# Optimization experiments

Measured on AMD Instinct MI355X. Metric: run time of the kernel, lower is better.

## Reference

```python
import jax, jax.numpy as jnp
import numpy as np

NCLS = 6
K = 2
ATOMS = 5          # ('vm','im','cm','sc','cc')
IN_DIM = 768
HID = 3072
NUM_PATCH = 576
B = 64
# Task t gates over 6 experts: [dense expert 0] + 5 atom-pair experts (a_in=t%5, a_out=0..4)
TASK_ATOM = [t % ATOMS for t in range(NCLS)]


def setup_inputs() -> dict:
    key = jax.random.key(0)
    ks = jax.random.split(key, 12)
    s = 0.02
    return {
        "x": jax.random.normal(ks[0], (B, NCLS + NUM_PATCH, IN_DIM), jnp.float32),
        "W1": jax.random.normal(ks[1], (IN_DIM, HID), jnp.float32) * s,
        "b1": jnp.zeros((HID,), jnp.float32),
        "W2": jax.random.normal(ks[2], (HID, IN_DIM), jnp.float32) * s,
        "b2": jnp.zeros((IN_DIM,), jnp.float32),
        "W_in": jax.random.normal(ks[3], (ATOMS, IN_DIM, HID), jnp.float32) * s,
        "b_in": jnp.zeros((ATOMS, HID), jnp.float32),
        "W_out": jax.random.normal(ks[4], (ATOMS, HID, IN_DIM), jnp.float32) * s,
        "b_out": jnp.zeros((ATOMS, IN_DIM), jnp.float32),
        "Wg": jax.random.normal(ks[5], (NCLS, IN_DIM, 6), jnp.float32) * s,
    }


def _gelu(x):
    return jax.nn.gelu(x, approximate=False)  # torch nn.GELU default (erf)


def reference(x, W1, b1, W2, b2, W_in, b_in, W_out, b_out, Wg):
    cls = x[:, :NCLS]                      # [B, ncls, d]
    patch = x[:, NCLS:]                    # [B, P, d]
    # dense FFN on patch tokens
    patch = _gelu(jnp.einsum('bpd,dh->bph', patch, W1) + b1)
    patch = jnp.einsum('bph,hd->bpd', patch, W2) + b2

    flat = cls.reshape(-1, cls.shape[-1])  # [N=B*ncls, d]
    # expert 0: the same dense FFN
    e0 = (_gelu(flat @ W1 + b1) @ W2 + b2).reshape(B, NCLS, IN_DIM)
    # atom-pair experts: shared hidden per atom_in, then each atom_out head
    hid = _gelu(jnp.einsum('nd,adh->anh', flat, W_in) + b_in[:, None, :])       # [5, N, H]
    allo = jnp.einsum('anh,ohd->aond', hid, W_out) + b_out[None, :, None, :]    # [5, 5, N, d]
    allo = allo.reshape(ATOMS, ATOMS, B, NCLS, IN_DIM)

    rows = jnp.arange(B)[:, None]
    mixed = []
    for t in range(NCLS):
        a = TASK_ATOM[t]
        g = jax.nn.softmax(cls[:, t] @ Wg[t], axis=-1)            # [B, 6]
        vals, idx = jax.lax.top_k(g, K)
        sparse = jnp.zeros_like(g).at[rows, idx].set(vals)
        g = sparse / jnp.maximum(sparse.sum(-1, keepdims=True), 1e-6)
        # selected experts in index order: [0, (a,0)..(a,4)]
        sel = jnp.concatenate(
            [e0[:, t][:, None, :], jnp.swapaxes(allo[a, :, :, t, :], 0, 1)], axis=1
        )                                                          # [B, 6, d]
        mixed.append(jnp.sum(sel * g[:, :, None], axis=1, keepdims=True))
    cls_out = jnp.concatenate(mixed, axis=1)                       # [B, ncls, d]
    return jnp.concatenate([cls_out, patch], axis=1)  # dropout is identity in eval
```

## Files before the change

### kernel.cpp

```cpp
#include <hip/hip_runtime.h>
#include <math.h>


typedef unsigned short bfu;
typedef __attribute__((ext_vector_type(8))) short bf16x8;
typedef __attribute__((ext_vector_type(4))) float f32x4;

#define GLD_LDS16(g, l)                                                        \
  __builtin_amdgcn_global_load_lds(                                            \
      (const __attribute__((address_space(1))) void*)(g),                      \
      (__attribute__((address_space(3))) void*)(l), 16, 0, 0)

__device__ __forceinline__ bfu f2bf(float f) {
  unsigned int u = __float_as_uint(f);
  u += 0x7FFFu + ((u >> 16) & 1u);
  return (bfu)(u >> 16);
}
__device__ __forceinline__ float gelu_exact(float v) {
  return 0.5f * v * (1.0f + erff(v * 0.70710678118654752440f));
}

template <int BM, int WC, int MF, int NF, bool GELU, bool OUTBF>
__device__ __forceinline__ void gemm_tile(
    bfu* As, bfu* Bs,
    const bfu* __restrict__ A,
    const bfu* __restrict__ Bt,
    const float* __restrict__ bias,
    void* __restrict__ out,
    int K, int ldo) {
  const int tid  = threadIdx.x;
  const int lane = tid & 63;
  const int wv   = tid >> 6;
  const int wm   = (wv / WC) * (MF * 16);
  const int wn   = (wv % WC) * (NF * 16);

  const f32x4 fzero = {0.f, 0.f, 0.f, 0.f};
  f32x4 acc[MF][NF];
#pragma unroll
  for (int m = 0; m < MF; ++m)
#pragma unroll
    for (int n = 0; n < NF; ++n) acc[m][n] = fzero;

  const int srow  = tid >> 3;
  const int gslot = (tid & 7) ^ (srow & 7);
  const bfu* ga = A  + (size_t)srow * K + gslot * 8;
  const bfu* gb = Bt + (size_t)srow * K + gslot * 8;

  const int lrow = lane & 15;
  const int lks  = lane >> 4;

  for (int kt = 0; kt < K; kt += 64) {
#pragma unroll
    for (int i = 0; i < BM / 32; ++i)
      GLD_LDS16(ga + kt + (size_t)i * 32 * K, As + i * 2048 + wv * 512);
#pragma unroll
    for (int i = 0; i < 4; ++i)
      GLD_LDS16(gb + kt + (size_t)i * 32 * K, Bs + i * 2048 + wv * 512);
    __syncthreads();

#pragma unroll
    for (int kk = 0; kk < 2; ++kk) {
      bf16x8 af[MF], bfr[NF];
#pragma unroll
      for (int m = 0; m < MF; ++m) {
        int row  = wm + m * 16 + lrow;
        int slot = (kk * 4 + lks) ^ (row & 7);
        af[m] = *(const bf16x8*)(As + row * 64 + slot * 8);
      }
#pragma unroll
      for (int n = 0; n < NF; ++n) {
        int row  = wn + n * 16 + lrow;
        int slot = (kk * 4 + lks) ^ (row & 7);
        bfr[n] = *(const bf16x8*)(Bs + row * 64 + slot * 8);
      }
#pragma unroll
      for (int m = 0; m < MF; ++m)
#pragma unroll
        for (int n = 0; n < NF; ++n)
          acc[m][n] = __builtin_amdgcn_mfma_f32_16x16x32_bf16(af[m], bfr[n],
                                                              acc[m][n], 0, 0, 0);
    }
    __syncthreads();
  }

  const int rbase = (lane >> 4) * 4;
#pragma unroll
  for (int n = 0; n < NF; ++n) {
    int col = wn + n * 16 + lrow;
    float bv = bias[col];
#pragma unroll
    for (int m = 0; m < MF; ++m) {
#pragma unroll
      for (int r = 0; r < 4; ++r) {
        int row = wm + m * 16 + rbase + r;
        float v = acc[m][n][r] + bv;
        if (GELU) v = gelu_exact(v);
        if (OUTBF)
          ((bfu*)out)[(size_t)row * ldo + col] = f2bf(v);
        else
          ((float*)out)[(size_t)row * ldo + col] = v;
      }
    }
  }
}

template <bool GELU, bool OUTBF>
__global__ __launch_bounds__(256) void gemm128_kernel(
    const bfu* __restrict__ A, const bfu* __restrict__ Bt,
    const float* __restrict__ bias, void* __restrict__ out, int K, int ldo) {
  __shared__ bfu As[128 * 64];
  __shared__ bfu Bs[128 * 64];
  size_t m0 = (size_t)blockIdx.x * 128, n0 = (size_t)blockIdx.y * 128;
  gemm_tile<128, 2, 4, 4, GELU, OUTBF>(
      As, Bs, A + m0 * K, Bt + n0 * K, bias + n0,
      (void*)((char*)out + ((size_t)m0 * ldo + n0) * (OUTBF ? 2 : 4)), K, ldo);
}

__global__ __launch_bounds__(256) void hidc_kernel(
    const bfu* __restrict__ clsb, const bfu* __restrict__ WinT,
    const float* __restrict__ b_in, bfu* __restrict__ hidc) {
  __shared__ bfu As[64 * 64];
  __shared__ bfu Bs[128 * 64];
  int t = blockIdx.y, a = t % 5, nt = blockIdx.x;
  gemm_tile<64, 4, 4, 2, true, true>(
      As, Bs, clsb + (size_t)t * 64 * 768,
      WinT + (size_t)a * 3072 * 768 + (size_t)nt * 128 * 768,
      b_in + a * 3072 + nt * 128,
      (void*)(hidc + (size_t)t * 64 * 3072 + nt * 128), 768, 3072);
}

__global__ __launch_bounds__(256) void allo_kernel(
    const bfu* __restrict__ hidc, const bfu* __restrict__ WoutT,
    const float* __restrict__ b_out, float* __restrict__ allo) {
  __shared__ bfu As[64 * 64];
  __shared__ bfu Bs[128 * 64];
  int t = blockIdx.y, nt = blockIdx.x;
  gemm_tile<64, 4, 4, 2, false, false>(
      As, Bs, hidc + (size_t)t * 64 * 3072,
      WoutT + (size_t)nt * 128 * 3072, b_out + nt * 128,
      (void*)(allo + (size_t)t * 64 * 3840 + nt * 128), 3072, 3840);
}

__global__ __launch_bounds__(256) void cvt_f32_bf16_kernel(
    const float* __restrict__ in, bfu* __restrict__ out, int n4) {
  int stride = gridDim.x * blockDim.x;
  for (int i = blockIdx.x * blockDim.x + threadIdx.x; i < n4; i += stride) {
    float4 v = ((const float4*)in)[i];
    ushort4 o;
    o.x = f2bf(v.x); o.y = f2bf(v.y); o.z = f2bf(v.z); o.w = f2bf(v.w);
    ((ushort4*)out)[i] = o;
  }
}

__global__ __launch_bounds__(256) void transpose_kernel(
    const float* __restrict__ in, bfu* __restrict__ out, int R, int C) {
  __shared__ float tile[32][33];
  int z = blockIdx.z;
  const float* src = in + (size_t)z * R * C;
  bfu* dst = out + (size_t)z * R * C;
  int c0 = blockIdx.x * 32, r0 = blockIdx.y * 32;
  int tx = threadIdx.x, ty = threadIdx.y;
#pragma unroll
  for (int j = 0; j < 32; j += 8)
    tile[ty + j][tx] = src[(size_t)(r0 + ty + j) * C + c0 + tx];
  __syncthreads();
#pragma unroll
  for (int j = 0; j < 32; j += 8)
    dst[(size_t)(c0 + ty + j) * R + r0 + tx] = f2bf(tile[tx][ty + j]);
}

__global__ __launch_bounds__(256) void build_clsb_kernel(
    const float* __restrict__ x, bfu* __restrict__ clsb) {
  int i = blockIdx.x * 256 + threadIdx.x;
  int d = i % 768, bt = i / 768;
  int b = bt % 64, t = bt / 64;
  clsb[i] = f2bf(x[((size_t)b * 582 + t) * 768 + d]);
}

__global__ __launch_bounds__(64) void gate_kernel(
    const float* __restrict__ x, const float* __restrict__ Wg,
    float* __restrict__ gw) {
  int bt = blockIdx.x;
  int b = bt / 6, t = bt % 6;
  const float* xr = x + ((size_t)b * 582 + t) * 768;
  const float* wg = Wg + (size_t)t * 768 * 6;
  int lane = threadIdx.x;
  float z[6] = {0.f, 0.f, 0.f, 0.f, 0.f, 0.f};
  for (int d = lane; d < 768; d += 64) {
    float xv = xr[d];
#pragma unroll
    for (int o = 0; o < 6; ++o) z[o] += xv * wg[d * 6 + o];
  }
#pragma unroll
  for (int o = 0; o < 6; ++o)
#pragma unroll
    for (int s = 32; s > 0; s >>= 1) z[o] += __shfl_down(z[o], s);
  if (lane == 0) {
    int i1 = 0;
#pragma unroll
    for (int o = 1; o < 6; ++o) if (z[o] > z[i1]) i1 = o;
    int i2 = -1;
#pragma unroll
    for (int o = 0; o < 6; ++o) {
      if (o == i1) continue;
      if (i2 < 0 || z[o] > z[i2]) i2 = o;
    }
    float w1 = 1.f / (1.f + expf(z[i2] - z[i1]));
    float o6[6] = {0.f, 0.f, 0.f, 0.f, 0.f, 0.f};
    o6[i1] = w1; o6[i2] = 1.f - w1;
#pragma unroll
    for (int o = 0; o < 6; ++o) gw[bt * 6 + o] = o6[o];
  }
}

__global__ __launch_bounds__(256) void mix_kernel(
    float* __restrict__ out, const float* __restrict__ allo,
    const float* __restrict__ gw) {
  int bt = blockIdx.x;
  int b = bt / 6, t = bt % 6;
  float g[6];
#pragma unroll
  for (int o = 0; o < 6; ++o) g[o] = gw[bt * 6 + o];
  float* orow = out + ((size_t)b * 582 + t) * 768;
  const float* arow = allo + ((size_t)t * 64 + b) * 3840;
  for (int d = threadIdx.x; d < 768; d += 256) {
    float v = g[0] * orow[d];
#pragma unroll
    for (int o = 0; o < 5; ++o) v += g[o + 1] * arow[o * 768 + d];
    orow[d] = v;
  }
}

extern "C" void kernel_launch(void* const* d_in, const int* in_sizes, int n_in,
                              void* d_out, int out_size, void* d_ws,
                              size_t ws_size, hipStream_t stream) {
  const float* x     = (const float*)d_in[0];
  const float* W1    = (const float*)d_in[1];
  const float* b1    = (const float*)d_in[2];
  const float* W2    = (const float*)d_in[3];
  const float* b2    = (const float*)d_in[4];
  const float* W_in  = (const float*)d_in[5];
  const float* b_in  = (const float*)d_in[6];
  const float* W_out = (const float*)d_in[7];
  const float* b_out = (const float*)d_in[8];
  const float* Wg    = (const float*)d_in[9];
  float* out = (float*)d_out;

  constexpr int M = 37248;
  constexpr int CHUNK_TILES = 97;
  constexpr int CHUNK_ROWS  = CHUNK_TILES * 128;
  constexpr size_t SZ_XB    = (size_t)M * 768 * 2;
  constexpr size_t SZ_W1T   = (size_t)3072 * 768 * 2;
  constexpr size_t SZ_W2T   = (size_t)768 * 3072 * 2;
  constexpr size_t SZ_WINT  = (size_t)5 * 3072 * 768 * 2;
  constexpr size_t SZ_WOUTT = (size_t)5 * 768 * 3072 * 2;
  constexpr size_t SZ_HID   = (size_t)CHUNK_ROWS * 3072 * 2;
  constexpr size_t SZ_CLSB  = (size_t)6 * 64 * 768 * 2;
  constexpr size_t SZ_HIDC  = (size_t)6 * 64 * 3072 * 2;
  constexpr size_t SZ_ALLO  = (size_t)6 * 64 * 3840 * 4;
  constexpr size_t SZ_GW    = (size_t)384 * 6 * 4;

  char* ws = (char*)d_ws;
  size_t off = 0;
  auto take = [&](size_t bytes) {
    char* p = ws + off;
    off += (bytes + 255) & ~(size_t)255;
    return p;
  };
  bfu*   xb    = (bfu*)take(SZ_XB);
  bfu*   W1t   = (bfu*)take(SZ_W1T);
  bfu*   W2t   = (bfu*)take(SZ_W2T);
  bfu*   WinT  = (bfu*)take(SZ_WINT);
  bfu*   WoutT = (bfu*)take(SZ_WOUTT);
  bfu*   hid   = (bfu*)take(SZ_HID);
  bfu*   clsb  = (bfu*)take(SZ_CLSB);
  bfu*   hidc  = (bfu*)take(SZ_HIDC);
  float* allo  = (float*)take(SZ_ALLO);
  float* gw    = (float*)take(SZ_GW);
  if (ws_size < off) return;

  cvt_f32_bf16_kernel<<<2048, 256, 0, stream>>>(x, xb, M * 768 / 4);
  transpose_kernel<<<dim3(96, 24, 1), dim3(32, 8), 0, stream>>>(W1, W1t, 768, 3072);
  transpose_kernel<<<dim3(24, 96, 1), dim3(32, 8), 0, stream>>>(W2, W2t, 3072, 768);
  transpose_kernel<<<dim3(96, 24, 5), dim3(32, 8), 0, stream>>>(W_in, WinT, 768, 3072);
  transpose_kernel<<<dim3(24, 96, 5), dim3(32, 8), 0, stream>>>(W_out, WoutT, 3072, 768);
  build_clsb_kernel<<<(6 * 64 * 768) / 256, 256, 0, stream>>>(x, clsb);
  gate_kernel<<<384, 64, 0, stream>>>(x, Wg, gw);

  for (int c = 0; c < 3; ++c) {
    const bfu* Ac = xb + (size_t)c * CHUNK_ROWS * 768;
    float* Oc = out + (size_t)c * CHUNK_ROWS * 768;
    gemm128_kernel<true, true><<<dim3(CHUNK_TILES, 24), 256, 0, stream>>>(
        Ac, W1t, b1, (void*)hid, 768, 3072);
    gemm128_kernel<false, false><<<dim3(CHUNK_TILES, 6), 256, 0, stream>>>(
        hid, W2t, b2, (void*)Oc, 3072, 768);
  }

  hidc_kernel<<<dim3(24, 6), 256, 0, stream>>>(clsb, WinT, b_in, hidc);
  allo_kernel<<<dim3(30, 6), 256, 0, stream>>>(hidc, WoutT, b_out, allo);
  mix_kernel<<<384, 256, 0, stream>>>(out, allo, gw);
}
```

Before: 1.123 ms.

## Replace 128x128 GEMM with pipelined 256x256 tile kernel and XCD-aware remap

Swaps the dense FFN GEMMs from 128x128 tiles with 256 threads to 256x256 tiles with 512 threads. The new kernel uses double-buffered LDS staging via global_load_lds split into per-k-half planes, explicit vmcnt waits and barriers, and s_setprio around the MFMA bursts, so loads overlap compute and each tile gets more reuse. Workgroup IDs are remapped so neighbouring tiles land on the same XCD, and the chunk boundaries are re-cut to 256-row multiples with a row bound check on the last chunk. The weight transposes are also merged into two launches. The risks are LDS and register pressure at 512 threads with a 128 KB LDS buffer, the subtle wait-count logic, and the last chunk reading past M rows of xb.

```diff
diff --git a/kernel.cpp b/kernel.cpp
--- a/kernel.cpp
+++ b/kernel.cpp
@@ -11,6 +11,9 @@
       (const __attribute__((address_space(1))) void*)(g),                      \
       (__attribute__((address_space(3))) void*)(l), 16, 0, 0)
 
+#define BAR() asm volatile("s_barrier" ::: "memory")
+#define VMW(n) asm volatile("s_waitcnt vmcnt(" #n ")" ::: "memory")
+
 __device__ __forceinline__ bfu f2bf(float f) {
   unsigned int u = __float_as_uint(f);
   u += 0x7FFFu + ((u >> 16) & 1u);
@@ -20,19 +23,154 @@
   return 0.5f * v * (1.0f + erff(v * 0.70710678118654752440f));
 }
 
+template <bool GELU, bool OUTBF>
+__global__ __launch_bounds__(512, 2) void gemm256_kernel(
+    const bfu* __restrict__ A, const bfu* __restrict__ Bt,
+    const float* __restrict__ bias, void* __restrict__ out, int K, int ldo,
+    int mrows) {
+  __shared__ bfu lds[8 * 8192];
+
+  const int tid = threadIdx.x;
+  const int lane = tid & 63;
+  const int wv = tid >> 6;
+  const int wm2 = wv >> 2;
+  const int wn4 = wv & 3;
+  const int lrow = lane & 15;
+  const int lks = lane >> 4;
+
+  int nwg = gridDim.x * gridDim.y;
+  int orig = blockIdx.y * gridDim.x + blockIdx.x;
+  int q = nwg >> 3, r = nwg & 7;
+  int xcd = orig & 7, loc = orig >> 3;
+  int w = (xcd < r) ? (xcd * (q + 1) + loc) : (r * (q + 1) + (xcd - r) * q + loc);
+  int bx = w % gridDim.x, by = w / gridDim.x;
+
+  const size_t m0 = (size_t)bx * 256;
+  const size_t n0 = (size_t)by * 256;
+  const bfu* Atile = A + m0 * K;
+  const bfu* Btile = Bt + n0 * K;
+
+  const int NT = K >> 6;
+  const int NPLANES = NT * 4;
+
+  int nextplane = 0;
+  auto STAGE = [&]() {
+    if (nextplane >= NPLANES) return;
+    int pidx = nextplane++;
+    int t = pidx >> 2, pl = pidx & 3;
+    int mat = pl & 1, kk = pl >> 1;
+    int buf = t & 1;
+    const bfu* src = mat ? Btile : Atile;
+    bfu* base = lds + (((((buf << 1) | mat) << 1) | kk) * 8192);
+    int kbase = t * 64 + kk * 32;
+#pragma unroll
+    for (int i = 0; i < 2; ++i) {
+      int idx = i * 512 + tid;
+      int row = idx >> 2, slot = idx & 3;
+      int gslot = slot ^ ((row >> 1) & 3);
+      GLD_LDS16(src + (size_t)row * K + kbase + gslot * 8,
+                base + i * 4096 + wv * 512);
+    }
+  };
+
+  const f32x4 fz = {0.f, 0.f, 0.f, 0.f};
+  f32x4 acc[8][4];
+#pragma unroll
+  for (int m = 0; m < 8; ++m)
+#pragma unroll
+    for (int n = 0; n < 4; ++n) acc[m][n] = fz;
+
+  for (int i = 0; i < 6; ++i) STAGE();
+  VMW(8);
+  BAR();
+
+  bf16x8 bfrag[4];
+  for (int t = 0; t < NT; ++t) {
+    const int buf = t & 1;
+#pragma unroll
+    for (int kk = 0; kk < 2; ++kk) {
+      const bfu* Ap = lds + (((((buf << 1) | 0) << 1) | kk) * 8192);
+      const bfu* Bp = lds + (((((buf << 1) | 1) << 1) | kk) * 8192);
+#pragma unroll
+      for (int h = 0; h < 2; ++h) {
+        bf16x8 af[4];
+        if (h == 0) {
+#pragma unroll
+          for (int n = 0; n < 4; ++n) {
+            int row = wn4 * 64 + n * 16 + lrow;
+            bfrag[n] =
+                *(const bf16x8*)(Bp + row * 32 + (lks ^ ((row >> 1) & 3)) * 8);
+          }
+        }
+#pragma unroll
+        for (int m = 0; m < 4; ++m) {
+          int row = wm2 * 128 + (h * 4 + m) * 16 + lrow;
+          af[m] =
+              *(const bf16x8*)(Ap + row * 32 + (lks ^ ((row >> 1) & 3)) * 8);
+        }
+        STAGE();
+        BAR();
+        __builtin_amdgcn_s_setprio(1);
+#pragma unroll
+        for (int m = 0; m < 4; ++m)
+#pragma unroll
+          for (int n = 0; n < 4; ++n)
+            acc[h * 4 + m][n] = __builtin_amdgcn_mfma_f32_16x16x32_bf16(
+                af[m], bfrag[n], acc[h * 4 + m][n], 0, 0, 0);
+        __builtin_amdgcn_s_setprio(0);
+        if (h == 1) {
+          if (kk == 0) {
+            if (t < NT - 1) {
+              VMW(8);
+            } else {
+              VMW(0);
+            }
+          } else {
+            if (t < NT - 2) {
+              VMW(8);
+            } else if (t == NT - 2) {
+              VMW(4);
+            }
+          }
+        }
+        BAR();
+      }
+    }
+  }
+
+  const int rbase = lks * 4;
+#pragma unroll
+  for (int n = 0; n < 4; ++n) {
+    int col = wn4 * 64 + n * 16 + lrow;
+    float bv = bias[n0 + col];
+#pragma unroll
+    for (int m = 0; m < 8; ++m) {
+#pragma unroll
+      for (int rr = 0; rr < 4; ++rr) {
+        int row = wm2 * 128 + m * 16 + rbase + rr;
+        if ((int)(m0 + row) < mrows) {
+          float v = acc[m][n][rr] + bv;
+          if (GELU) v = gelu_exact(v);
+          size_t o = (m0 + row) * (size_t)ldo + (n0 + col);
+          if (OUTBF)
+            ((bfu*)out)[o] = f2bf(v);
+          else
+            ((float*)out)[o] = v;
+        }
+      }
+    }
+  }
+}
+
 template <int BM, int WC, int MF, int NF, bool GELU, bool OUTBF>
 __device__ __forceinline__ void gemm_tile(
-    bfu* As, bfu* Bs,
-    const bfu* __restrict__ A,
-    const bfu* __restrict__ Bt,
-    const float* __restrict__ bias,
-    void* __restrict__ out,
-    int K, int ldo) {
-  const int tid  = threadIdx.x;
+    bfu* As, bfu* Bs, const bfu* __restrict__ A, const bfu* __restrict__ Bt,
+    const float* __restrict__ bias, void* __restrict__ out, int K, int ldo) {
+  const int tid = threadIdx.x;
   const int lane = tid & 63;
-  const int wv   = tid >> 6;
-  const int wm   = (wv / WC) * (MF * 16);
-  const int wn   = (wv % WC) * (NF * 16);
+  const int wv = tid >> 6;
+  const int wm = (wv / WC) * (MF * 16);
+  const int wn = (wv % WC) * (NF * 16);
 
   const f32x4 fzero = {0.f, 0.f, 0.f, 0.f};
   f32x4 acc[MF][NF];
@@ -41,13 +179,13 @@
 #pragma unroll
     for (int n = 0; n < NF; ++n) acc[m][n] = fzero;
 
-  const int srow  = tid >> 3;
+  const int srow = tid >> 3;
   const int gslot = (tid & 7) ^ (srow & 7);
-  const bfu* ga = A  + (size_t)srow * K + gslot * 8;
+  const bfu* ga = A + (size_t)srow * K + gslot * 8;
   const bfu* gb = Bt + (size_t)srow * K + gslot * 8;
 
   const int lrow = lane & 15;
-  const int lks  = lane >> 4;
+  const int lks = lane >> 4;
 
   for (int kt = 0; kt < K; kt += 64) {
 #pragma unroll
@@ -63,13 +201,13 @@
       bf16x8 af[MF], bfr[NF];
 #pragma unroll
       for (int m = 0; m < MF; ++m) {
-        int row  = wm + m * 16 + lrow;
+        int row = wm + m * 16 + lrow;
         int slot = (kk * 4 + lks) ^ (row & 7);
         af[m] = *(const bf16x8*)(As + row * 64 + slot * 8);
       }
 #pragma unroll
       for (int n = 0; n < NF; ++n) {
-        int row  = wn + n * 16 + lrow;
+        int row = wn + n * 16 + lrow;
         int slot = (kk * 4 + lks) ^ (row & 7);
         bfr[n] = *(const bf16x8*)(Bs + row * 64 + slot * 8);
       }
@@ -102,18 +240,6 @@
       }
     }
   }
-}
-
-template <bool GELU, bool OUTBF>
-__global__ __launch_bounds__(256) void gemm128_kernel(
-    const bfu* __restrict__ A, const bfu* __restrict__ Bt,
-    const float* __restrict__ bias, void* __restrict__ out, int K, int ldo) {
-  __shared__ bfu As[128 * 64];
-  __shared__ bfu Bs[128 * 64];
-  size_t m0 = (size_t)blockIdx.x * 128, n0 = (size_t)blockIdx.y * 128;
-  gemm_tile<128, 2, 4, 4, GELU, OUTBF>(
-      As, Bs, A + m0 * K, Bt + n0 * K, bias + n0,
-      (void*)((char*)out + ((size_t)m0 * ldo + n0) * (OUTBF ? 2 : 4)), K, ldo);
 }
 
 __global__ __launch_bounds__(256) void hidc_kernel(
@@ -152,12 +278,13 @@
   }
 }
 
-__global__ __launch_bounds__(256) void transpose_kernel(
-    const float* __restrict__ in, bfu* __restrict__ out, int R, int C) {
+__global__ __launch_bounds__(256) void transpose2_kernel(
+    const float* __restrict__ s0, const float* __restrict__ s1,
+    bfu* __restrict__ d0, bfu* __restrict__ d1, int R, int C) {
   __shared__ float tile[32][33];
   int z = blockIdx.z;
-  const float* src = in + (size_t)z * R * C;
-  bfu* dst = out + (size_t)z * R * C;
+  const float* src = (z == 0) ? s0 : s1 + (size_t)(z - 1) * R * C;
+  bfu* dst = (z == 0) ? d0 : d1 + (size_t)(z - 1) * R * C;
   int c0 = blockIdx.x * 32, r0 = blockIdx.y * 32;
   int tx = threadIdx.x, ty = threadIdx.y;
 #pragma unroll
@@ -234,31 +361,29 @@
 extern "C" void kernel_launch(void* const* d_in, const int* in_sizes, int n_in,
                               void* d_out, int out_size, void* d_ws,
                               size_t ws_size, hipStream_t stream) {
-  const float* x     = (const float*)d_in[0];
-  const float* W1    = (const float*)d_in[1];
-  const float* b1    = (const float*)d_in[2];
-  const float* W2    = (const float*)d_in[3];
-  const float* b2    = (const float*)d_in[4];
-  const float* W_in  = (const float*)d_in[5];
-  const float* b_in  = (const float*)d_in[6];
+  const float* x = (const float*)d_in[0];
+  const float* W1 = (const float*)d_in[1];
+  const float* b1 = (const float*)d_in[2];
+  const float* W2 = (const float*)d_in[3];
+  const float* b2 = (const float*)d_in[4];
+  const float* W_in = (const float*)d_in[5];
+  const float* b_in = (const float*)d_in[6];
   const float* W_out = (const float*)d_in[7];
   const float* b_out = (const float*)d_in[8];
-  const float* Wg    = (const float*)d_in[9];
+  const float* Wg = (const float*)d_in[9];
   float* out = (float*)d_out;
 
   constexpr int M = 37248;
-  constexpr int CHUNK_TILES = 97;
-  constexpr int CHUNK_ROWS  = CHUNK_TILES * 128;
-  constexpr size_t SZ_XB    = (size_t)M * 768 * 2;
-  constexpr size_t SZ_W1T   = (size_t)3072 * 768 * 2;
-  constexpr size_t SZ_W2T   = (size_t)768 * 3072 * 2;
-  constexpr size_t SZ_WINT  = (size_t)5 * 3072 * 768 * 2;
+  constexpr size_t SZ_XB = (size_t)M * 768 * 2;
+  constexpr size_t SZ_W1T = (size_t)3072 * 768 * 2;
+  constexpr size_t SZ_W2T = (size_t)768 * 3072 * 2;
+  constexpr size_t SZ_WINT = (size_t)5 * 3072 * 768 * 2;
   constexpr size_t SZ_WOUTT = (size_t)5 * 768 * 3072 * 2;
-  constexpr size_t SZ_HID   = (size_t)CHUNK_ROWS * 3072 * 2;
-  constexpr size_t SZ_CLSB  = (size_t)6 * 64 * 768 * 2;
-  constexpr size_t SZ_HIDC  = (size_t)6 * 64 * 3072 * 2;
-  constexpr size_t SZ_ALLO  = (size_t)6 * 64 * 3840 * 4;
-  constexpr size_t SZ_GW    = (size_t)384 * 6 * 4;
+  constexpr size_t SZ_HID = (size_t)12544 * 3072 * 2;
+  constexpr size_t SZ_CLSB = (size_t)6 * 64 * 768 * 2;
+  constexpr size_t SZ_HIDC = (size_t)6 * 64 * 3072 * 2;
+  constexpr size_t SZ_ALLO = (size_t)6 * 64 * 3840 * 4;
+  constexpr size_t SZ_GW = (size_t)384 * 6 * 4;
 
   char* ws = (char*)d_ws;
   size_t off = 0;
@@ -267,33 +392,36 @@
     off += (bytes + 255) & ~(size_t)255;
     return p;
   };
-  bfu*   xb    = (bfu*)take(SZ_XB);
-  bfu*   W1t   = (bfu*)take(SZ_W1T);
-  bfu*   W2t   = (bfu*)take(SZ_W2T);
-  bfu*   WinT  = (bfu*)take(SZ_WINT);
-  bfu*   WoutT = (bfu*)take(SZ_WOUTT);
-  bfu*   hid   = (bfu*)take(SZ_HID);
-  bfu*   clsb  = (bfu*)take(SZ_CLSB);
-  bfu*   hidc  = (bfu*)take(SZ_HIDC);
-  float* allo  = (float*)take(SZ_ALLO);
-  float* gw    = (float*)take(SZ_GW);
+  bfu* xb = (bfu*)take(SZ_XB);
+  bfu* W1t = (bfu*)take(SZ_W1T);
+  bfu* W2t = (bfu*)take(SZ_W2T);
+  bfu* WinT = (bfu*)take(SZ_WINT);
+  bfu* WoutT = (bfu*)take(SZ_WOUTT);
+  bfu* hid = (bfu*)take(SZ_HID);
+  bfu* clsb = (bfu*)take(SZ_CLSB);
+  bfu* hidc = (bfu*)take(SZ_HIDC);
+  float* allo = (float*)take(SZ_ALLO);
+  float* gw = (float*)take(SZ_GW);
   if (ws_size < off) return;
 
   cvt_f32_bf16_kernel<<<2048, 256, 0, stream>>>(x, xb, M * 768 / 4);
-  transpose_kernel<<<dim3(96, 24, 1), dim3(32, 8), 0, stream>>>(W1, W1t, 768, 3072);
-  transpose_kernel<<<dim3(24, 96, 1), dim3(32, 8), 0, stream>>>(W2, W2t, 3072, 768);
-  transpose_kernel<<<dim3(96, 24, 5), dim3(32, 8), 0, stream>>>(W_in, WinT, 768, 3072);
-  transpose_kernel<<<dim3(24, 96, 5), dim3(32, 8), 0, stream>>>(W_out, WoutT, 3072, 768);
+  transpose2_kernel<<<dim3(96, 24, 6), dim3(32, 8), 0, stream>>>(
+      W1, W_in, W1t, WinT, 768, 3072);
+  transpose2_kernel<<<dim3(24, 96, 6), dim3(32, 8), 0, stream>>>(
+      W2, W_out, W2t, WoutT, 3072, 768);
   build_clsb_kernel<<<(6 * 64 * 768) / 256, 256, 0, stream>>>(x, clsb);
   gate_kernel<<<384, 64, 0, stream>>>(x, Wg, gw);
 
+  const int cstart[4] = {0, 12544, 25088, 37376};
   for (int c = 0; c < 3; ++c) {
-    const bfu* Ac = xb + (size_t)c * CHUNK_ROWS * 768;
-    float* Oc = out + (size_t)c * CHUNK_ROWS * 768;
-    gemm128_kernel<true, true><<<dim3(CHUNK_TILES, 24), 256, 0, stream>>>(
-        Ac, W1t, b1, (void*)hid, 768, 3072);
-    gemm128_kernel<false, false><<<dim3(CHUNK_TILES, 6), 256, 0, stream>>>(
-        hid, W2t, b2, (void*)Oc, 3072, 768);
+    int start = cstart[c];
+    int alloc = cstart[c + 1] - start;
+    int mtiles = alloc / 256;
+    int valid = M - start < alloc ? M - start : alloc;
+    gemm256_kernel<true, true><<<dim3(mtiles, 12), 512, 0, stream>>>(
+        xb + (size_t)start * 768, W1t, b1, (void*)hid, 768, 3072, valid);
+    gemm256_kernel<false, false><<<dim3(mtiles, 3), 512, 0, stream>>>(
+        hid, W2t, b2, (void*)(out + (size_t)start * 768), 3072, 768, valid);
   }
 
   hidc_kernel<<<dim3(24, 6), 256, 0, stream>>>(clsb, WinT, b_in, hidc);
```

Result: slower. 1.299 ms (+15.6%).
